# Kernel tuning notes

Measured on AMD Instinct MI355X. Metric: run time of the kernel, lower is better.

Reference implementation:

```python
import jax, jax.numpy as jnp
import numpy as np

B, S, H = 4, 1024, 1024
NHEADS = 16
DK = H // NHEADS


def setup_inputs() -> dict:
    key = jax.random.key(0)
    ks = jax.random.split(key, 9)
    scale = 1.0 / np.sqrt(H).astype(np.float32)
    query = jax.random.normal(ks[0], (B, S, H), dtype=jnp.float32)
    key_in = jax.random.normal(ks[1], (B, S, H), dtype=jnp.float32)
    score_mask = jax.random.randint(ks[2], (B, S, S), 0, 2).astype(bool)
    # torch nn.Linear params, stored as [in, out] so y = x @ W + b
    Wq = jax.random.normal(ks[3], (H, H), dtype=jnp.float32) * scale
    bq = jax.random.normal(ks[4], (H,), dtype=jnp.float32) * scale
    Wk = jax.random.normal(ks[5], (H, H), dtype=jnp.float32) * scale
    bk = jax.random.normal(ks[6], (H,), dtype=jnp.float32) * scale
    Wp = jax.random.normal(ks[7], (H, H), dtype=jnp.float32) * scale
    bp = jax.random.normal(ks[8], (H,), dtype=jnp.float32) * scale
    return dict(query=query, key_in=key_in, score_mask=score_mask,
                Wq=Wq, bq=bq, Wk=Wk, bk=bk, Wp=Wp, bp=bp)


def reference(query, key_in, score_mask, Wq, bq, Wk, bk, Wp, bp):
    # Projections + head split: [B,S,H] -> [B,h,S,dk]
    q = (query @ Wq + bq).reshape(B, S, NHEADS, DK).transpose(0, 2, 1, 3)
    k = (key_in @ Wk + bk).reshape(B, S, NHEADS, DK).transpose(0, 2, 1, 3)
    inv_sqrt_dk = jnp.asarray(1.0 / np.sqrt(DK), dtype=q.dtype)
    scores = jnp.einsum('bhqd,bhkd->bhqk', q, k) * inv_sqrt_dk
    # masked_fill(score_mask.unsqueeze(1), -1e9): mask True = masked, broadcast over heads
    scores = jnp.where(score_mask[:, None, :, :], jnp.asarray(-1e9, scores.dtype), scores)
    # redundant per-row mask multiply: b = ~mask[:, None, :, 0:1]
    row_keep = (~score_mask[:, None, :, 0:1]).astype(scores.dtype)  # [B,1,S,1]
    p_attn = jax.nn.softmax(scores, axis=-1) * row_keep
    # NON-STANDARD: value is the projected query, not a separate value tensor
    out = jnp.einsum('bhqk,bhkd->bhqd', p_attn, q)
    out = out.transpose(0, 2, 1, 3).reshape(B, S, H)  # merge heads
    return out @ Wp + bp
```

## Files before the change

### kernel.cpp

```cpp
#include <hip/hip_runtime.h>
#include <hip/hip_bf16.h>

using bf16x8 = __attribute__((ext_vector_type(8))) short;
using f32x4  = __attribute__((ext_vector_type(4))) float;

static __device__ __forceinline__ short f2bf(float f) {
  union { float f; unsigned u; } x; x.f = f;
  unsigned r = x.u + 0x7fffu + ((x.u >> 16) & 1u);
  return (short)(r >> 16);
}
static __device__ __forceinline__ float bf2f(short b) {
  union { unsigned u; float f; } x; x.u = ((unsigned)(unsigned short)b) << 16;
  return x.f;
}
static __device__ __forceinline__ unsigned pack_bf2(float lo, float hi) {
  __hip_bfloat162 h = __float22bfloat162_rn(float2{lo, hi});
  unsigned u; __builtin_memcpy(&u, &h, 4); return u;
}
static __device__ __forceinline__ float exp2_raw(float x) {
  float r; asm("v_exp_f32 %0, %1" : "=v"(r) : "v"(x)); return r;
}
static __device__ __forceinline__ void gll16(const void* g, void* l) {
  __builtin_amdgcn_global_load_lds((__attribute__((address_space(1))) const void*)g,
                                   (__attribute__((address_space(3))) void*)l, 16, 0, 0);
}

__global__ void k_prep(const float* __restrict__ query, const float* __restrict__ key_in,
                       const float* __restrict__ Wq, const float* __restrict__ Wk,
                       const float* __restrict__ Wp,
                       const unsigned* __restrict__ mask_u32,
                       short* __restrict__ Qbf, short* __restrict__ Kbf,
                       short* __restrict__ Wt3, unsigned long long* __restrict__ packb) {
  const int bid = blockIdx.x, tid = threadIdx.x;
  if (bid < 2048) {
    const float* in = bid < 1024 ? query : key_in;
    short* out = bid < 1024 ? Qbf : Kbf;
    const int r = bid & 1023;
    const int n4 = (4 * 1024 * 1024) / 4;
    for (int i = r * 256 + tid; i < n4; i += 1024 * 256) {
      float4 v = reinterpret_cast<const float4*>(in)[i];
      short4 o;
      o.x = f2bf(v.x); o.y = f2bf(v.y); o.z = f2bf(v.z); o.w = f2bf(v.w);
      reinterpret_cast<short4*>(out)[i] = o;
    }
  } else if (bid < 5120) {
    __shared__ float tile[32][33];
    const int sub = bid - 2048;
    const int w = sub >> 10, s2 = sub & 1023;
    const int bx = s2 & 31, by = s2 >> 5;
    const float* in = w == 0 ? Wq : (w == 1 ? Wk : Wp);
    short* out = Wt3 + (size_t)w * 1024 * 1024;
    const int tx = tid & 31, ty = tid >> 5;
    int x = bx * 32 + tx, y0 = by * 32;
    for (int j = 0; j < 32; j += 8)
      tile[ty + j][tx] = in[(size_t)(y0 + ty + j) * 1024 + x];
    __syncthreads();
    int xo = by * 32 + tx, yo = bx * 32;
    for (int j = 0; j < 32; j += 8)
      out[(size_t)(yo + ty + j) * 1024 + xo] = f2bf(tile[tx][ty + j]);
  } else {
    const int r = bid - 5120;
    unsigned probe = mask_u32[tid & 63];
    const bool u8mode = (__ballot(probe > 1u) != 0ull);
    const unsigned char* s8 = (const unsigned char*)mask_u32;
    const int* s32 = (const int*)mask_u32;
    const int n = 4 * 1024 * 1024;
    for (int e = r * 256 + tid; e < n; e += 2048 * 256) {
      int v = u8mode ? (int)s8[e] : s32[e];
      unsigned long long b = __ballot(v != 0);
      if ((tid & 63) == 0) packb[e >> 6] = b;
    }
  }
}

template<int OUT_BF16, int BN, int M, int N, int K, int VT_OUT>
__device__ __forceinline__ void gemm_body(const short* __restrict__ A,
                                          const short* __restrict__ Bt,
                                          const float* __restrict__ bias,
                                          void* __restrict__ C,
                                          short* __restrict__ Vtg,
                                          short* __restrict__ Al,
                                          short* __restrict__ Bl) {
  constexpr int JF = BN / 32;
  const int tid  = threadIdx.x;
  const int lane = tid & 63, wid = tid >> 6;
  const int g = lane >> 4, lr = lane & 15;
  const int wm = wid >> 1, wn = wid & 1;
  constexpr int nbx = N / BN;
  constexpr int nwg = nbx * (M >> 7);
  const int lin = blockIdx.y * nbx + blockIdx.x;
  const int orig = (lin & 7) * (nwg >> 3) + (lin >> 3);
  const int m0 = (orig / nbx) * 128, n0 = (orig % nbx) * BN;
  const int srow = lane >> 3;
  const int sch  = ((lane & 7) ^ srow) * 8;

  f32x4 acc[4][JF];
#pragma unroll
  for (int i = 0; i < 4; ++i)
#pragma unroll
    for (int j = 0; j < JF; ++j) acc[i][j] = (f32x4){0.f, 0.f, 0.f, 0.f};

  constexpr int NT = K >> 6;
  auto stage = [&](int buf, int kt) {
#pragma unroll
    for (int s = 0; s < 4; ++s)
      gll16(&A[(size_t)(m0 + s * 32 + wid * 8 + srow) * K + kt + sch],
            &Al[buf * 128 * 64 + (s * 32 + wid * 8) * 64]);
#pragma unroll
    for (int s = 0; s < BN / 32; ++s)
      gll16(&Bt[(size_t)(n0 + s * 32 + wid * 8 + srow) * K + kt + sch],
            &Bl[buf * BN * 64 + (s * 32 + wid * 8) * 64]);
  };

  stage(0, 0);
  asm volatile("s_waitcnt vmcnt(0)" ::: "memory");
  __builtin_amdgcn_s_barrier();
  asm volatile("" ::: "memory");

#pragma unroll 1
  for (int t = 0; t < NT; ++t) {
    const int cur = t & 1;
    if (t + 1 < NT) stage(cur ^ 1, (t + 1) * 64);
#pragma unroll
    for (int kb = 0; kb < 2; ++kb) {
      const int cs = ((kb * 4 + g) ^ (lr & 7)) * 8;
      bf16x8 af[4], bfr[JF];
#pragma unroll
      for (int i = 0; i < 4; ++i)
        af[i] = *reinterpret_cast<const bf16x8*>(
            &Al[cur * 128 * 64 + (wm * 64 + i * 16 + lr) * 64 + cs]);
#pragma unroll
      for (int j = 0; j < JF; ++j)
        bfr[j] = *reinterpret_cast<const bf16x8*>(
            &Bl[cur * BN * 64 + (wn * (BN / 2) + j * 16 + lr) * 64 + cs]);
#pragma unroll
      for (int i = 0; i < 4; ++i)
#pragma unroll
        for (int j = 0; j < JF; ++j)
          acc[i][j] = __builtin_amdgcn_mfma_f32_16x16x32_bf16(af[i], bfr[j], acc[i][j], 0, 0, 0);
    }
    if (t + 1 < NT) {
      asm volatile("s_waitcnt vmcnt(0)" ::: "memory");
      __builtin_amdgcn_s_barrier();
      asm volatile("" ::: "memory");
    }
  }

#pragma unroll
  for (int i = 0; i < 4; ++i) {
    int row = m0 + wm * 64 + i * 16 + g * 4;
#pragma unroll
    for (int j = 0; j < JF; ++j) {
      int col = n0 + wn * (BN / 2) + j * 16 + lr;
      float bv = bias[col];
#pragma unroll
      for (int r = 0; r < 4; ++r) {
        float v = acc[i][j][r] + bv;
        if (OUT_BF16) ((short*)C)[(size_t)(row + r) * N + col] = f2bf(v);
        else          ((float*)C)[(size_t)(row + r) * N + col] = v;
      }
    }
  }

  if (VT_OUT) {
    short* T = Al;
    __builtin_amdgcn_s_barrier();
    asm volatile("" ::: "memory");
#pragma unroll
    for (int i = 0; i < 4; ++i) {
      int row = wm * 64 + i * 16 + g * 4;
#pragma unroll
      for (int j = 0; j < JF; ++j) {
        int col = wn * (BN / 2) + j * 16 + lr;
        float bv = bias[n0 + col];
        unsigned d0 = pack_bf2(acc[i][j][0] + bv, acc[i][j][1] + bv);
        unsigned d1 = pack_bf2(acc[i][j][2] + bv, acc[i][j][3] + bv);
        unsigned long long w = (unsigned long long)d0 | ((unsigned long long)d1 << 32);
        *reinterpret_cast<unsigned long long*>(
            &T[col * 128 + (row ^ ((col & 7) << 4))]) = w;
      }
    }
    __builtin_amdgcn_s_barrier();
    asm volatile("" ::: "memory");
    const int bb = m0 >> 10, s0 = m0 & 1023, h0 = n0 >> 6;
#pragma unroll
    for (int it = 0; it < 8; ++it) {
      int ch = it * 256 + tid;
      int d_loc = ch >> 4, sc = ch & 15;
      bf16x8 v = *reinterpret_cast<const bf16x8*>(
          &T[d_loc * 128 + ((sc * 8) ^ ((d_loc & 7) << 4))]);
      *reinterpret_cast<bf16x8*>(
          &Vtg[(size_t)((bb * 16 + h0 + (d_loc >> 6)) * 64 + (d_loc & 63)) * 1024
               + s0 + sc * 8]) = v;
    }
  }
}

__launch_bounds__(256)
__global__ void k_gemm_qk(const short* __restrict__ A0, const short* __restrict__ A1,
                          const short* __restrict__ Bt3,
                          const float* __restrict__ b0, const float* __restrict__ b1,
                          short* __restrict__ C0, short* __restrict__ C1,
                          short* __restrict__ Vtg) {
  __shared__ short Al[2][128 * 64];
  __shared__ short Bl[2][128 * 64];
  if (blockIdx.z == 0)
    gemm_body<1, 128, 4096, 1024, 1024, 1>(A0, Bt3, b0, C0, Vtg,
                                           &Al[0][0], &Bl[0][0]);
  else
    gemm_body<1, 128, 4096, 1024, 1024, 0>(A1, Bt3 + 1024 * 1024, b1, C1, nullptr,
                                           &Al[0][0], &Bl[0][0]);
}

__launch_bounds__(256)
__global__ void k_gemm_out(const short* __restrict__ A, const short* __restrict__ Bt,
                           const float* __restrict__ bias, float* __restrict__ C) {
  __shared__ short Al[2][128 * 64];
  __shared__ short Bl[2][64 * 64];
  gemm_body<0, 64, 4096, 1024, 1024, 0>(A, Bt, bias, C, nullptr,
                                        &Al[0][0], &Bl[0][0]);
}

__launch_bounds__(512)
__global__ void k_attention(const short* __restrict__ Qp, const short* __restrict__ Kp,
                            const short* __restrict__ Vtg,
                            const unsigned long long* __restrict__ mb,
                            short* __restrict__ O) {
  __shared__ short Kl[3][64 * 64];
  __shared__ short Vl[3][64 * 64];
  __shared__ short Pl[8][16 * 64];
  const int tid  = threadIdx.x;
  const int lane = tid & 63, wid = tid >> 6;
  const int g = lane >> 4, lr = lane & 15;
  const int g4 = 4 * g;
  const int bid = (blockIdx.x & 7) * 64 + (blockIdx.x >> 3);
  const int qt = bid & 7, h = (bid >> 3) & 15, b = bid >> 7;
  const int qb = qt * 128 + wid * 16;
  const int srow = lane >> 3;
  const int sch  = ((lane & 7) ^ srow) * 8;

  const size_t qrow = (size_t)(b * 1024 + qb + lr);
  const float qs = 0.125f * 1.44269504088896340736f;
  bf16x8 aq[2];
#pragma unroll
  for (int db = 0; db < 2; ++db) {
    bf16x8 raw = *reinterpret_cast<const bf16x8*>(&Qp[qrow * 1024 + h * 64 + db * 32 + g * 8]);
#pragma unroll
    for (int j = 0; j < 8; j += 2) {
      unsigned pk = pack_bf2(bf2f(raw[j]) * qs, bf2f(raw[j + 1]) * qs);
      aq[db][j]     = (short)(pk & 0xffffu);
      aq[db][j + 1] = (short)(pk >> 16);
    }
  }

  const unsigned long long* mrow = &mb[qrow * 16];
  const short* Ksrc = &Kp[(size_t)(b * 1024 + wid * 8 + srow) * 1024 + h * 64 + sch];
  const short* Vsrc = &Vtg[(size_t)((b * 16 + h) * 64 + wid * 8 + srow) * 1024 + sch];

  f32x4 o[4];
#pragma unroll
  for (int d = 0; d < 4; ++d) o[d] = (f32x4){0.f, 0.f, 0.f, 0.f};
  float l_part = 0.f;
  short* Prow = &Pl[wid][lr * 64];

  gll16(Ksrc,                     &Kl[0][(wid * 8) * 64]);
  gll16(Vsrc,                     &Vl[0][(wid * 8) * 64]);
  gll16(Ksrc + (size_t)64 * 1024, &Kl[1][(wid * 8) * 64]);
  gll16(Vsrc + 64,                &Vl[1][(wid * 8) * 64]);
  unsigned long long mwA = mrow[0];
  unsigned long long mwB = mrow[1];
  unsigned long long mwC = 0;
  const float keep = (mwA & 1ull) ? 0.f : 1.f;

  int cur = 0;
  int b2  = 2;
#pragma unroll 1
  for (int kt = 0; kt < 16; ++kt) {
    if (kt >= 1) {
      const short* Vb = Vl[b2];
      __builtin_amdgcn_s_setprio(1);
#pragma unroll
      for (int kb = 0; kb < 2; ++kb) {
        bf16x8 pa = *reinterpret_cast<const bf16x8*>(
            &Prow[(((kb * 4 + g) ^ (lr & 7)) * 8)]);
        const int cs = ((kb * 4 + g) ^ (lr & 7)) * 8;
#pragma unroll
        for (int d = 0; d < 4; ++d) {
          bf16x8 vf = *reinterpret_cast<const bf16x8*>(&Vb[(d * 16 + lr) * 64 + cs]);
          o[d] = __builtin_amdgcn_mfma_f32_16x16x32_bf16(vf, pa, o[d], 0, 0, 0);
        }
      }
      __builtin_amdgcn_s_setprio(0);
    }

    if (kt < 15) asm volatile("s_waitcnt vmcnt(4)" ::: "memory");
    else         asm volatile("s_waitcnt vmcnt(0)" ::: "memory");
    __builtin_amdgcn_s_barrier();
    asm volatile("" ::: "memory");

    if (kt + 2 < 16) {
      gll16(Ksrc + (size_t)(kt + 2) * 64 * 1024, &Kl[b2][(wid * 8) * 64]);
      gll16(Vsrc + (kt + 2) * 64,                &Vl[b2][(wid * 8) * 64]);
      mwC = mrow[kt + 2];
    }

    const unsigned mlo = (unsigned)mwA;
    const unsigned mhi = (unsigned)(mwA >> 32);

#pragma unroll
    for (int kc = 0; kc < 4; ++kc) {
      f32x4 a = (f32x4){0.f, 0.f, 0.f, 0.f};
      __builtin_amdgcn_s_setprio(1);
#pragma unroll
      for (int db = 0; db < 2; ++db) {
        bf16x8 kf = *reinterpret_cast<const bf16x8*>(
            &Kl[cur][(kc * 16 + lr) * 64 + (((db * 4 + g) ^ (lr & 7)) * 8)]);
        a = __builtin_amdgcn_mfma_f32_16x16x32_bf16(kf, aq[db], a, 0, 0, 0);
      }
      __builtin_amdgcn_s_setprio(0);
      const unsigned wk = ((kc < 2 ? mlo : mhi) >> (((kc & 1) << 4) + g4)) & 0xFu;
      float p0 = (wk & 1u) ? 0.f : exp2_raw(a[0]);
      float p1 = (wk & 2u) ? 0.f : exp2_raw(a[1]);
      float p2 = (wk & 4u) ? 0.f : exp2_raw(a[2]);
      float p3 = (wk & 8u) ? 0.f : exp2_raw(a[3]);
      l_part += (p0 + p1) + (p2 + p3);
      unsigned lo = pack_bf2(p0, p1), hi = pack_bf2(p2, p3);
      unsigned long long w = (unsigned long long)lo | ((unsigned long long)hi << 32);
      *reinterpret_cast<unsigned long long*>(
          &Prow[((2 * kc + (g >> 1)) ^ (lr & 7)) * 8 + (g & 1) * 4]) = w;
    }
    mwA = mwB; mwB = mwC;
    cur = (cur == 2) ? 0 : cur + 1;
    b2  = (b2  == 2) ? 0 : b2  + 1;
    asm volatile("" ::: "memory");
  }

  {
    const short* Vb = Vl[0];
    __builtin_amdgcn_s_setprio(1);
#pragma unroll
    for (int kb = 0; kb < 2; ++kb) {
      bf16x8 pa = *reinterpret_cast<const bf16x8*>(
          &Prow[(((kb * 4 + g) ^ (lr & 7)) * 8)]);
      const int cs = ((kb * 4 + g) ^ (lr & 7)) * 8;
#pragma unroll
      for (int d = 0; d < 4; ++d) {
        bf16x8 vf = *reinterpret_cast<const bf16x8*>(&Vb[(d * 16 + lr) * 64 + cs]);
        o[d] = __builtin_amdgcn_mfma_f32_16x16x32_bf16(vf, pa, o[d], 0, 0, 0);
      }
    }
    __builtin_amdgcn_s_setprio(0);
  }

  float l_run = l_part;
  l_run += __shfl_xor(l_run, 16);
  l_run += __shfl_xor(l_run, 32);

  const float inv = (l_run > 0.f) ? keep / l_run : 0.f;
#pragma unroll
  for (int d = 0; d < 4; ++d) {
    unsigned lo = pack_bf2(o[d][0] * inv, o[d][1] * inv);
    unsigned hi = pack_bf2(o[d][2] * inv, o[d][3] * inv);
    unsigned long long w = (unsigned long long)lo | ((unsigned long long)hi << 32);
    *reinterpret_cast<unsigned long long*>(
        &Prow[((2 * d + (g >> 1)) ^ (lr & 7)) * 8 + (g & 1) * 4]) = w;
  }
#pragma unroll
  for (int it = 0; it < 2; ++it) {
    int qq = it * 8 + srow;
    bf16x8 val = *reinterpret_cast<const bf16x8*>(
        &Pl[wid][qq * 64 + (((lane & 7) ^ (qq & 7)) * 8)]);
    *reinterpret_cast<bf16x8*>(
        &O[(size_t)(b * 1024 + qt * 128 + wid * 16 + qq) * 1024 + h * 64 + (lane & 7) * 8]) = val;
  }
}

extern "C" void kernel_launch(void* const* d_in, const int* in_sizes, int n_in,
                              void* d_out, int out_size, void* d_ws, size_t ws_size,
                              hipStream_t stream) {
  const float* query  = (const float*)d_in[0];
  const float* key_in = (const float*)d_in[1];
  const void*  mask_raw = d_in[2];
  const float* Wq = (const float*)d_in[3];
  const float* bq = (const float*)d_in[4];
  const float* Wk = (const float*)d_in[5];
  const float* bk = (const float*)d_in[6];
  const float* Wp = (const float*)d_in[7];
  const float* bp = (const float*)d_in[8];

  char* ws = (char*)d_ws;
  size_t off = 0;
  auto alloc = [&](size_t bytes) {
    char* p = ws + off;
    off = (off + bytes + 255) & ~(size_t)255;
    return p;
  };
  unsigned long long* packb = (unsigned long long*)alloc(512ull << 10);
  short* Qbf   = (short*)alloc(8ull << 20);
  short* Kbf   = (short*)alloc(8ull << 20);
  short* Wt3   = (short*)alloc(6ull << 20);
  short* Qproj = (short*)alloc(8ull << 20);
  short* Kproj = (short*)alloc(8ull << 20);
  short* Vtg   = (short*)alloc(8ull << 20);
  short* AttnO = Kbf;

  k_prep<<<7168, 256, 0, stream>>>(query, key_in, Wq, Wk, Wp,
                                   (const unsigned*)mask_raw, Qbf, Kbf, Wt3, packb);

  dim3 gqk(8, 32, 2);
  k_gemm_qk<<<gqk, 256, 0, stream>>>(Qbf, Kbf, Wt3, bq, bk, Qproj, Kproj, Vtg);

  k_attention<<<512, 512, 0, stream>>>(Qproj, Kproj, Vtg, packb, AttnO);

  k_gemm_out<<<dim3(16, 32), 256, 0, stream>>>(AttnO, Wt3 + 2 * 1024 * 1024, bp,
                                               (float*)d_out);
}
```

Measured before the change: 96.96 us.

## Process 128-key tiles per barrier with double-buffered K/V staging

```diff
diff --git a/kernel.cpp b/kernel.cpp
--- a/kernel.cpp
+++ b/kernel.cpp
@@ -226,8 +226,8 @@
                             const short* __restrict__ Vtg,
                             const unsigned long long* __restrict__ mb,
                             short* __restrict__ O) {
-  __shared__ short Kl[3][64 * 64];
-  __shared__ short Vl[3][64 * 64];
+  __shared__ short Kl[2][2][64 * 64];
+  __shared__ short Vl[2][2][64 * 64];
   __shared__ short Pl[8][16 * 64];
   const int tid  = threadIdx.x;
   const int lane = tid & 63, wid = tid >> 6;
@@ -263,21 +263,63 @@
   float l_part = 0.f;
   short* Prow = &Pl[wid][lr * 64];
 
-  gll16(Ksrc,                     &Kl[0][(wid * 8) * 64]);
-  gll16(Vsrc,                     &Vl[0][(wid * 8) * 64]);
-  gll16(Ksrc + (size_t)64 * 1024, &Kl[1][(wid * 8) * 64]);
-  gll16(Vsrc + 64,                &Vl[1][(wid * 8) * 64]);
-  unsigned long long mwA = mrow[0];
-  unsigned long long mwB = mrow[1];
-  unsigned long long mwC = 0;
-  const float keep = (mwA & 1ull) ? 0.f : 1.f;
-
-  int cur = 0;
-  int b2  = 2;
+  gll16(Ksrc,                           &Kl[0][0][(wid * 8) * 64]);
+  gll16(Ksrc + (size_t)64 * 1024,       &Kl[0][1][(wid * 8) * 64]);
+  gll16(Vsrc,                           &Vl[0][0][(wid * 8) * 64]);
+  gll16(Vsrc + 64,                      &Vl[0][1][(wid * 8) * 64]);
+  unsigned long long mwA0 = mrow[0], mwA1 = mrow[1];
+  unsigned long long mwB0 = 0, mwB1 = 0;
+  const float keep = (mwA0 & 1ull) ? 0.f : 1.f;
+
 #pragma unroll 1
-  for (int kt = 0; kt < 16; ++kt) {
-    if (kt >= 1) {
-      const short* Vb = Vl[b2];
+  for (int kt = 0; kt < 8; ++kt) {
+    const int cur = kt & 1;
+    if (kt < 7) asm volatile("s_waitcnt vmcnt(2)" ::: "memory");
+    else        asm volatile("s_waitcnt vmcnt(0)" ::: "memory");
+    __builtin_amdgcn_s_barrier();
+    asm volatile("" ::: "memory");
+
+    if (kt + 1 < 8) {
+      const size_t kb128 = (size_t)(kt + 1) * 128;
+      gll16(Ksrc + kb128 * 1024,              &Kl[cur ^ 1][0][(wid * 8) * 64]);
+      gll16(Ksrc + (kb128 + 64) * 1024,       &Kl[cur ^ 1][1][(wid * 8) * 64]);
+      gll16(Vsrc + kb128,                     &Vl[cur ^ 1][0][(wid * 8) * 64]);
+      gll16(Vsrc + kb128 + 64,                &Vl[cur ^ 1][1][(wid * 8) * 64]);
+      mwB0 = mrow[2 * kt + 2];
+      mwB1 = mrow[2 * kt + 3];
+    }
+
+#pragma unroll
+    for (int hk = 0; hk < 2; ++hk) {
+      const unsigned long long mwfull = hk ? mwA1 : mwA0;
+      const unsigned mlo = (unsigned)mwfull;
+      const unsigned mhi = (unsigned)(mwfull >> 32);
+      const short* Kb = Kl[cur][hk];
+      const short* Vb = Vl[cur][hk];
+
+#pragma unroll
+      for (int kc = 0; kc < 4; ++kc) {
+        f32x4 a = (f32x4){0.f, 0.f, 0.f, 0.f};
+        __builtin_amdgcn_s_setprio(1);
+#pragma unroll
+        for (int db = 0; db < 2; ++db) {
+          bf16x8 kf = *reinterpret_cast<const bf16x8*>(
+              &Kb[(kc * 16 + lr) * 64 + (((db * 4 + g) ^ (lr & 7)) * 8)]);
+          a = __builtin_amdgcn_mfma_f32_16x16x32_bf16(kf, aq[db], a, 0, 0, 0);
+        }
+        __builtin_amdgcn_s_setprio(0);
+        const unsigned wk = ((kc < 2 ? mlo : mhi) >> (((kc & 1) << 4) + g4)) & 0xFu;
+        float p0 = (wk & 1u) ? 0.f : exp2_raw(a[0]);
+        float p1 = (wk & 2u) ? 0.f : exp2_raw(a[1]);
+        float p2 = (wk & 4u) ? 0.f : exp2_raw(a[2]);
+        float p3 = (wk & 8u) ? 0.f : exp2_raw(a[3]);
+        l_part += (p0 + p1) + (p2 + p3);
+        unsigned lo = pack_bf2(p0, p1), hi = pack_bf2(p2, p3);
+        unsigned long long w = (unsigned long long)lo | ((unsigned long long)hi << 32);
+        *reinterpret_cast<unsigned long long*>(
+            &Prow[((2 * kc + (g >> 1)) ^ (lr & 7)) * 8 + (g & 1) * 4]) = w;
+      }
+
       __builtin_amdgcn_s_setprio(1);
 #pragma unroll
       for (int kb = 0; kb < 2; ++kb) {
@@ -292,64 +334,8 @@
       }
       __builtin_amdgcn_s_setprio(0);
     }
-
-    if (kt < 15) asm volatile("s_waitcnt vmcnt(4)" ::: "memory");
-    else         asm volatile("s_waitcnt vmcnt(0)" ::: "memory");
-    __builtin_amdgcn_s_barrier();
+    mwA0 = mwB0; mwA1 = mwB1;
     asm volatile("" ::: "memory");
-
-    if (kt + 2 < 16) {
-      gll16(Ksrc + (size_t)(kt + 2) * 64 * 1024, &Kl[b2][(wid * 8) * 64]);
-      gll16(Vsrc + (kt + 2) * 64,                &Vl[b2][(wid * 8) * 64]);
-      mwC = mrow[kt + 2];
-    }
-
-    const unsigned mlo = (unsigned)mwA;
-    const unsigned mhi = (unsigned)(mwA >> 32);
-
-#pragma unroll
-    for (int kc = 0; kc < 4; ++kc) {
-      f32x4 a = (f32x4){0.f, 0.f, 0.f, 0.f};
-      __builtin_amdgcn_s_setprio(1);
-#pragma unroll
-      for (int db = 0; db < 2; ++db) {
-        bf16x8 kf = *reinterpret_cast<const bf16x8*>(
-            &Kl[cur][(kc * 16 + lr) * 64 + (((db * 4 + g) ^ (lr & 7)) * 8)]);
-        a = __builtin_amdgcn_mfma_f32_16x16x32_bf16(kf, aq[db], a, 0, 0, 0);
-      }
-      __builtin_amdgcn_s_setprio(0);
-      const unsigned wk = ((kc < 2 ? mlo : mhi) >> (((kc & 1) << 4) + g4)) & 0xFu;
-      float p0 = (wk & 1u) ? 0.f : exp2_raw(a[0]);
-      float p1 = (wk & 2u) ? 0.f : exp2_raw(a[1]);
-      float p2 = (wk & 4u) ? 0.f : exp2_raw(a[2]);
-      float p3 = (wk & 8u) ? 0.f : exp2_raw(a[3]);
-      l_part += (p0 + p1) + (p2 + p3);
-      unsigned lo = pack_bf2(p0, p1), hi = pack_bf2(p2, p3);
-      unsigned long long w = (unsigned long long)lo | ((unsigned long long)hi << 32);
-      *reinterpret_cast<unsigned long long*>(
-          &Prow[((2 * kc + (g >> 1)) ^ (lr & 7)) * 8 + (g & 1) * 4]) = w;
-    }
-    mwA = mwB; mwB = mwC;
-    cur = (cur == 2) ? 0 : cur + 1;
-    b2  = (b2  == 2) ? 0 : b2  + 1;
-    asm volatile("" ::: "memory");
-  }
-
-  {
-    const short* Vb = Vl[0];
-    __builtin_amdgcn_s_setprio(1);
-#pragma unroll
-    for (int kb = 0; kb < 2; ++kb) {
-      bf16x8 pa = *reinterpret_cast<const bf16x8*>(
-          &Prow[(((kb * 4 + g) ^ (lr & 7)) * 8)]);
-      const int cs = ((kb * 4 + g) ^ (lr & 7)) * 8;
-#pragma unroll
-      for (int d = 0; d < 4; ++d) {
-        bf16x8 vf = *reinterpret_cast<const bf16x8*>(&Vb[(d * 16 + lr) * 64 + cs]);
-        o[d] = __builtin_amdgcn_mfma_f32_16x16x32_bf16(vf, pa, o[d], 0, 0, 0);
-      }
-    }
-    __builtin_amdgcn_s_setprio(0);
   }
 
   float l_run = l_part;
```

Result: faster. 93.23 us (median of 2 runs) (-3.8%).

## Shrink attention blocks to 4 waves and double-buffer K/V tiles

Applied to the files above, without the earlier changes.

```diff
diff --git a/kernel.cpp b/kernel.cpp
--- a/kernel.cpp
+++ b/kernel.cpp
@@ -221,21 +221,21 @@
                                         &Al[0][0], &Bl[0][0]);
 }
 
-__launch_bounds__(512)
+__launch_bounds__(256)
 __global__ void k_attention(const short* __restrict__ Qp, const short* __restrict__ Kp,
                             const short* __restrict__ Vtg,
                             const unsigned long long* __restrict__ mb,
                             short* __restrict__ O) {
-  __shared__ short Kl[3][64 * 64];
-  __shared__ short Vl[3][64 * 64];
-  __shared__ short Pl[8][16 * 64];
+  __shared__ short Kl[2][64 * 64];
+  __shared__ short Vl[2][64 * 64];
+  __shared__ short Pl[4][16 * 64];
   const int tid  = threadIdx.x;
   const int lane = tid & 63, wid = tid >> 6;
   const int g = lane >> 4, lr = lane & 15;
   const int g4 = 4 * g;
-  const int bid = (blockIdx.x & 7) * 64 + (blockIdx.x >> 3);
-  const int qt = bid & 7, h = (bid >> 3) & 15, b = bid >> 7;
-  const int qb = qt * 128 + wid * 16;
+  const int bid = (blockIdx.x & 7) * 128 + (blockIdx.x >> 3);
+  const int qt = bid & 15, h = (bid >> 4) & 15, b = bid >> 8;
+  const int qb = qt * 64 + wid * 16;
   const int srow = lane >> 3;
   const int sch  = ((lane & 7) ^ srow) * 8;
 
@@ -263,49 +263,37 @@
   float l_part = 0.f;
   short* Prow = &Pl[wid][lr * 64];
 
-  gll16(Ksrc,                     &Kl[0][(wid * 8) * 64]);
-  gll16(Vsrc,                     &Vl[0][(wid * 8) * 64]);
-  gll16(Ksrc + (size_t)64 * 1024, &Kl[1][(wid * 8) * 64]);
-  gll16(Vsrc + 64,                &Vl[1][(wid * 8) * 64]);
+  gll16(Ksrc,                           &Kl[0][(wid * 8) * 64]);
+  gll16(Ksrc + (size_t)32 * 1024,       &Kl[0][(32 + wid * 8) * 64]);
+  gll16(Vsrc,                           &Vl[0][(wid * 8) * 64]);
+  gll16(Vsrc + (size_t)32 * 1024,       &Vl[0][(32 + wid * 8) * 64]);
   unsigned long long mwA = mrow[0];
   unsigned long long mwB = mrow[1];
   unsigned long long mwC = 0;
   const float keep = (mwA & 1ull) ? 0.f : 1.f;
 
-  int cur = 0;
-  int b2  = 2;
 #pragma unroll 1
   for (int kt = 0; kt < 16; ++kt) {
-    if (kt >= 1) {
-      const short* Vb = Vl[b2];
-      __builtin_amdgcn_s_setprio(1);
-#pragma unroll
-      for (int kb = 0; kb < 2; ++kb) {
-        bf16x8 pa = *reinterpret_cast<const bf16x8*>(
-            &Prow[(((kb * 4 + g) ^ (lr & 7)) * 8)]);
-        const int cs = ((kb * 4 + g) ^ (lr & 7)) * 8;
-#pragma unroll
-        for (int d = 0; d < 4; ++d) {
-          bf16x8 vf = *reinterpret_cast<const bf16x8*>(&Vb[(d * 16 + lr) * 64 + cs]);
-          o[d] = __builtin_amdgcn_mfma_f32_16x16x32_bf16(vf, pa, o[d], 0, 0, 0);
-        }
-      }
-      __builtin_amdgcn_s_setprio(0);
-    }
-
-    if (kt < 15) asm volatile("s_waitcnt vmcnt(4)" ::: "memory");
+    const int cur = kt & 1;
+    if (kt < 15) asm volatile("s_waitcnt vmcnt(1)" ::: "memory");
     else         asm volatile("s_waitcnt vmcnt(0)" ::: "memory");
     __builtin_amdgcn_s_barrier();
     asm volatile("" ::: "memory");
 
-    if (kt + 2 < 16) {
-      gll16(Ksrc + (size_t)(kt + 2) * 64 * 1024, &Kl[b2][(wid * 8) * 64]);
-      gll16(Vsrc + (kt + 2) * 64,                &Vl[b2][(wid * 8) * 64]);
-      mwC = mrow[kt + 2];
+    if (kt + 1 < 16) {
+      const short* Ks = Ksrc + (size_t)(kt + 1) * 64 * 1024;
+      const short* Vs = Vsrc + (kt + 1) * 64;
+      gll16(Ks,                      &Kl[cur ^ 1][(wid * 8) * 64]);
+      gll16(Ks + (size_t)32 * 1024,  &Kl[cur ^ 1][(32 + wid * 8) * 64]);
+      gll16(Vs,                      &Vl[cur ^ 1][(wid * 8) * 64]);
+      gll16(Vs + (size_t)32 * 1024,  &Vl[cur ^ 1][(32 + wid * 8) * 64]);
+      if (kt + 2 < 16) mwC = mrow[kt + 2];
     }
 
     const unsigned mlo = (unsigned)mwA;
     const unsigned mhi = (unsigned)(mwA >> 32);
+    const short* Kb = Kl[cur];
+    const short* Vb = Vl[cur];
 
 #pragma unroll
     for (int kc = 0; kc < 4; ++kc) {
@@ -314,7 +302,7 @@
 #pragma unroll
       for (int db = 0; db < 2; ++db) {
         bf16x8 kf = *reinterpret_cast<const bf16x8*>(
-            &Kl[cur][(kc * 16 + lr) * 64 + (((db * 4 + g) ^ (lr & 7)) * 8)]);
+            &Kb[(kc * 16 + lr) * 64 + (((db * 4 + g) ^ (lr & 7)) * 8)]);
         a = __builtin_amdgcn_mfma_f32_16x16x32_bf16(kf, aq[db], a, 0, 0, 0);
       }
       __builtin_amdgcn_s_setprio(0);
@@ -329,14 +317,7 @@
       *reinterpret_cast<unsigned long long*>(
           &Prow[((2 * kc + (g >> 1)) ^ (lr & 7)) * 8 + (g & 1) * 4]) = w;
     }
-    mwA = mwB; mwB = mwC;
-    cur = (cur == 2) ? 0 : cur + 1;
-    b2  = (b2  == 2) ? 0 : b2  + 1;
-    asm volatile("" ::: "memory");
-  }
-
-  {
-    const short* Vb = Vl[0];
+
     __builtin_amdgcn_s_setprio(1);
 #pragma unroll
     for (int kb = 0; kb < 2; ++kb) {
@@ -350,6 +331,9 @@
       }
     }
     __builtin_amdgcn_s_setprio(0);
+
+    mwA = mwB; mwB = mwC;
+    asm volatile("" ::: "memory");
   }
 
   float l_run = l_part;
@@ -371,7 +355,7 @@
     bf16x8 val = *reinterpret_cast<const bf16x8*>(
         &Pl[wid][qq * 64 + (((lane & 7) ^ (qq & 7)) * 8)]);
     *reinterpret_cast<bf16x8*>(
-        &O[(size_t)(b * 1024 + qt * 128 + wid * 16 + qq) * 1024 + h * 64 + (lane & 7) * 8]) = val;
+        &O[(size_t)(b * 1024 + qt * 64 + wid * 16 + qq) * 1024 + h * 64 + (lane & 7) * 8]) = val;
   }
 }
 
@@ -410,7 +394,7 @@
   dim3 gqk(8, 32, 2);
   k_gemm_qk<<<gqk, 256, 0, stream>>>(Qbf, Kbf, Wt3, bq, bk, Qproj, Kproj, Vtg);
 
-  k_attention<<<512, 512, 0, stream>>>(Qproj, Kproj, Vtg, packb, AttnO);
+  k_attention<<<1024, 256, 0, stream>>>(Qproj, Kproj, Vtg, packb, AttnO);
 
   k_gemm_out<<<dim3(16, 32), 256, 0, stream>>>(AttnO, Wt3 + 2 * 1024 * 1024, bp,
                                                (float*)d_out);
```

Result: no change. 97.43 us (+0.5%).
